# Kernel tuning notes

Hardware: AMD Instinct MI355X
Metric: run time of the kernel (lower is better)

The kernel has to match this reference:

```python
import jax, jax.numpy as jnp
import numpy as np


def setup_inputs() -> dict:
    key = jax.random.key(0)
    k1, k2 = jax.random.split(key)
    B, C, H, W = 8, 64, 64, 64
    x = jax.random.normal(k1, (B, C, H, W), dtype=jnp.float32)
    stdv = 1.0 / np.sqrt(C)
    weight = jax.random.uniform(k2, (C, C), dtype=jnp.float32, minval=-stdv, maxval=stdv)
    return {"x": x, "weight": weight}


def reference(x, weight):
    B, C, H, W = x.shape
    N = H * W
    xf = x.reshape(B, C, N)            # [B, C, N]
    g_x = jnp.transpose(xf, (0, 2, 1))  # [B, N, C] (also theta_x)
    # f[b, i, j] = sum_c x[b, c, i] * x[b, c, j]
    f = jnp.einsum('bic,bcj->bij', g_x, xf)  # [B, N, N]
    adj = jax.nn.softmax(f, axis=-1)
    support = jnp.einsum('bnc,cd->bnd', g_x, weight)  # [B, N, C]
    y = jnp.einsum('bij,bjc->bic', adj, support)      # [B, N, C]
    y = jnp.transpose(y, (0, 2, 1)).reshape(B, C, H, W)
    return y + x
```

## Files before the change

### kernel.cpp

```cpp
#include <hip/hip_runtime.h>
#include <stdint.h>


#define NTOK 4096
#define CCH  64
#define LOG2E 1.44269504088896340736f

typedef float v4f __attribute__((ext_vector_type(4)));
typedef __bf16 v8bf __attribute__((ext_vector_type(8)));
typedef unsigned short v8us __attribute__((ext_vector_type(8)));

__device__ __forceinline__ unsigned short f2bf(float f) {
    union { float f; unsigned int u; } c; c.f = f;
    unsigned int r = c.u + 0x7fffu + ((c.u >> 16) & 1u);
    return (unsigned short)(r >> 16);
}

__device__ __forceinline__ v8bf ld8(const unsigned short* p) {
    union { v8us s; v8bf b; } u;
    u.s = *(const v8us*)p;
    return u.b;
}

__device__ __forceinline__ unsigned int pkbf(float a, float b) {
    union { float f; unsigned int u; } ua, ub; ua.f = a; ub.f = b;
    return __builtin_amdgcn_perm(ub.u, ua.u, 0x07060302u);
}

__device__ __forceinline__ void gload_lds16(const void* g, void* l) {
    __builtin_amdgcn_global_load_lds(
        (const __attribute__((address_space(1))) unsigned int*)g,
        (__attribute__((address_space(3))) unsigned int*)l,
        16, 0, 0);
}

__global__ __launch_bounds__(256) void prep_kernel(
    const float* __restrict__ x,
    const float* __restrict__ w,
    unsigned short* __restrict__ xT,
    unsigned short* __restrict__ sT)
{
    __shared__ float Xf[64 * 65];
    __shared__ __align__(16) unsigned short Xb[64 * 64];

    const int tid  = threadIdx.x;
    const int lane = tid & 63;
    const int wv   = __builtin_amdgcn_readfirstlane(tid >> 6);
    const int quad = lane >> 4;
    const int l16  = lane & 15;
    const int b    = blockIdx.y;
    const int n0   = blockIdx.x * 64;

    const float* xb = x + (size_t)b * CCH * NTOK + n0 + lane;
    #pragma unroll
    for (int k = 0; k < 16; ++k) {
        const int c = wv * 16 + k;
        Xf[c * 65 + lane] = xb[(size_t)c * NTOK];
    }
    __syncthreads();

    {
        const int n  = tid >> 2;
        const int c0 = (tid & 3) * 16;
        unsigned int pk[8];
        #pragma unroll
        for (int k = 0; k < 8; ++k) {
            const float a  = Xf[(c0 + 2 * k) * 65 + n];
            const float c2 = Xf[(c0 + 2 * k + 1) * 65 + n];
            pk[k] = (unsigned int)f2bf(a) | ((unsigned int)f2bf(c2) << 16);
        }
        unsigned short* xtr = xT + ((size_t)b * NTOK + n0 + n) * CCH + c0;
        *(uint4*)(xtr)     = *(uint4*)(pk);
        *(uint4*)(xtr + 8) = *(uint4*)(pk + 4);
        const int g0 = c0 >> 3;
        *(uint4*)(Xb + (n << 6) + ((g0 ^ (n & 7)) << 3))       = *(uint4*)(pk);
        *(uint4*)(Xb + (n << 6) + (((g0 + 1) ^ (n & 7)) << 3)) = *(uint4*)(pk + 4);
    }
    __syncthreads();

    v8bf aw0[4], aw1[4];
    #pragma unroll
    for (int dt = 0; dt < 4; ++dt) {
        #pragma unroll
        for (int j = 0; j < 8; ++j) {
            aw0[dt][j] = (__bf16)w[(quad * 8 + j) * 64 + dt * 16 + l16];
            aw1[dt][j] = (__bf16)w[(quad * 8 + j + 32) * 64 + dt * 16 + l16];
        }
    }
    const int nrow = wv * 16 + l16;
    const unsigned short* xr = Xb + (nrow << 6);
    const int cc = quad ^ (nrow & 7);
    const v8bf bx0 = ld8(xr + (cc << 3));
    const v8bf bx1 = ld8(xr + ((cc ^ 4) << 3));

    unsigned short* stb = sT + (size_t)b * CCH * NTOK + n0 + wv * 16 + l16;
    #pragma unroll
    for (int dt = 0; dt < 4; ++dt) {
        v4f z; z[0]=0.f; z[1]=0.f; z[2]=0.f; z[3]=0.f;
        z = __builtin_amdgcn_mfma_f32_16x16x32_bf16(aw0[dt], bx0, z, 0, 0, 0);
        z = __builtin_amdgcn_mfma_f32_16x16x32_bf16(aw1[dt], bx1, z, 0, 0, 0);
        #pragma unroll
        for (int r = 0; r < 4; ++r)
            stb[(size_t)(dt * 16 + quad * 4 + r) * NTOK] = f2bf(z[r]);
    }
}

__global__ __launch_bounds__(256, 4) void flash_kernel(
    const unsigned short* __restrict__ xT,
    const unsigned short* __restrict__ sT,
    float* __restrict__ part_o,
    float* __restrict__ part_l,
    int nchunk, int chunk_len)
{
    __shared__ __align__(16) unsigned short Kt[64 * 64];
    __shared__ __align__(16) unsigned short Vt[64 * 64];
    __shared__ __align__(16) unsigned short Pt[4][32 * 64];

    const int tid  = threadIdx.x;
    const int w    = tid >> 6;
    const int lane = tid & 63;
    const int quad = lane >> 4;
    const int l16  = lane & 15;
    const int l7   = l16 & 7;
    const int b     = blockIdx.z;
    const int chunk = blockIdx.y;
    const int i0   = blockIdx.x * 128;
    const int irow = i0 + w * 32;
    const int jb   = chunk * chunk_len;

    const unsigned short* xTb = xT + (size_t)b * NTOK * CCH;
    const unsigned short* sTb = sT + (size_t)b * CCH * NTOK;

    const int srow = w * 8 + (lane >> 3);
    const int sc   = (lane & 7) ^ (lane >> 3);
    unsigned short* kd0 = Kt + w * 512;
    unsigned short* vd0 = Vt + w * 512;

    v8bf aq0[2], aq1[2];
    #pragma unroll
    for (int m = 0; m < 2; ++m) {
        const unsigned short* qr = xTb + (size_t)(irow + m * 16 + l16) * CCH + quad * 8;
        aq0[m] = ld8(qr);
        aq1[m] = ld8(qr + 32);
    }

    float negml2[2];
    #pragma unroll
    for (int m = 0; m < 2; ++m) {
        float msq = 0.f;
        #pragma unroll
        for (int i = 0; i < 8; ++i) {
            float e0 = (float)aq0[m][i], e1 = (float)aq1[m][i];
            msq = fmaf(e0, e0, msq);
            msq = fmaf(e1, e1, msq);
        }
        msq += __shfl_xor(msq, 16);
        msq += __shfl_xor(msq, 32);
        negml2[m] = -msq * LOG2E;
    }

    v8bf ones;
    #pragma unroll
    for (int i = 0; i < 8; ++i) ones[i] = (__bf16)1.0f;

    v4f o[2][4];
    v4f lsum[2];
    #pragma unroll
    for (int m = 0; m < 2; ++m) {
        lsum[m][0]=0.f; lsum[m][1]=0.f; lsum[m][2]=0.f; lsum[m][3]=0.f;
        #pragma unroll
        for (int ct = 0; ct < 4; ++ct) { o[m][ct][0]=0.f; o[m][ct][1]=0.f; o[m][ct][2]=0.f; o[m][ct][3]=0.f; }
    }

    unsigned short* Pw = Pt[w];
    const int phalf = (quad & 1) * 4;
    const int pgq   = quad >> 1;

    for (int jj = 0; jj < chunk_len; jj += 64) {
        const int j0 = jb + jj;

        gload_lds16(xTb + (size_t)(j0 + srow) * CCH + sc * 8,       kd0);
        gload_lds16(xTb + (size_t)(j0 + 32 + srow) * CCH + sc * 8,  kd0 + 2048);
        gload_lds16(sTb + (size_t)srow * NTOK + j0 + sc * 8,        vd0);
        gload_lds16(sTb + (size_t)(32 + srow) * NTOK + j0 + sc * 8, vd0 + 2048);
        __syncthreads();

        #pragma unroll
        for (int jt = 0; jt < 4; ++jt) {
            const int krow = 16 * jt + l16;
            const unsigned short* kb = Kt + krow * 64;
            const int c0 = quad ^ (krow & 7);
            v8bf bk0 = ld8(kb + c0 * 8);
            v8bf bk1 = ld8(kb + (c0 ^ 4) * 8);
            #pragma unroll
            for (int m = 0; m < 2; ++m) {
                v4f z; z[0]=0.f; z[1]=0.f; z[2]=0.f; z[3]=0.f;
                z = __builtin_amdgcn_mfma_f32_16x16x32_bf16(bk0, aq0[m], z, 0, 0, 0);
                z = __builtin_amdgcn_mfma_f32_16x16x32_bf16(bk1, aq1[m], z, 0, 0, 0);
                const float p0 = exp2f(fmaf(z[0], LOG2E, negml2[m]));
                const float p1 = exp2f(fmaf(z[1], LOG2E, negml2[m]));
                const float p2 = exp2f(fmaf(z[2], LOG2E, negml2[m]));
                const float p3 = exp2f(fmaf(z[3], LOG2E, negml2[m]));
                uint2 pk; pk.x = pkbf(p0, p1); pk.y = pkbf(p2, p3);
                const int pos = (2 * jt + pgq) ^ l7;
                *(uint2*)(Pw + (m * 16 + l16) * 64 + pos * 8 + phalf) = pk;
            }
        }

        v8bf pb0[2], pb1[2];
        #pragma unroll
        for (int m = 0; m < 2; ++m) {
            const unsigned short* pr = Pw + (m * 16 + l16) * 64;
            const int p0c = quad ^ l7;
            pb0[m] = ld8(pr + p0c * 8);
            pb1[m] = ld8(pr + (p0c ^ 4) * 8);
            lsum[m] = __builtin_amdgcn_mfma_f32_16x16x32_bf16(ones, pb0[m], lsum[m], 0, 0, 0);
            lsum[m] = __builtin_amdgcn_mfma_f32_16x16x32_bf16(ones, pb1[m], lsum[m], 0, 0, 0);
        }

        #pragma unroll
        for (int ct = 0; ct < 4; ++ct) {
            const int vrow = 16 * ct + l16;
            const unsigned short* vb = Vt + vrow * 64;
            const int c0 = quad ^ (vrow & 7);
            v8bf bv0 = ld8(vb + c0 * 8);
            v8bf bv1 = ld8(vb + (c0 ^ 4) * 8);
            #pragma unroll
            for (int m = 0; m < 2; ++m) {
                o[m][ct] = __builtin_amdgcn_mfma_f32_16x16x32_bf16(bv0, pb0[m], o[m][ct], 0, 0, 0);
                o[m][ct] = __builtin_amdgcn_mfma_f32_16x16x32_bf16(bv1, pb1[m], o[m][ct], 0, 0, 0);
            }
        }
        __syncthreads();
    }

    const size_t pbase = (size_t)(b * nchunk + chunk) * NTOK + irow;
    #pragma unroll
    for (int m = 0; m < 2; ++m)
        if (quad == 0) part_l[pbase + m * 16 + l16] = lsum[m][0];
    float* po = part_o + pbase * 64;
    #pragma unroll
    for (int m = 0; m < 2; ++m)
        #pragma unroll
        for (int ct = 0; ct < 4; ++ct)
            *(v4f*)(po + (size_t)(m * 16 + l16) * 64 + ct * 16 + quad * 4) = o[m][ct];
}

template <int KS_>
__global__ __launch_bounds__(256) void combine_kernel(
    const float* __restrict__ part_o,
    const float* __restrict__ part_l,
    const float* __restrict__ x,
    float* __restrict__ out)
{
    __shared__ float Of[32 * 65];
    const int tid = threadIdx.x;
    const int b = blockIdx.y;
    const int i0 = blockIdx.x * 32;

    const int row = tid >> 3;
    const int col = (tid & 7) * 8;
    float acc[8];
    #pragma unroll
    for (int k = 0; k < 8; ++k) acc[k] = 0.f;
    float lt = 0.f;

    #pragma unroll
    for (int ch = 0; ch < KS_; ++ch) {
        const size_t base = (size_t)(b * KS_ + ch) * NTOK + i0 + row;
        lt += part_l[base];
        const float* po = part_o + base * 64 + col;
        float4 v0 = *(const float4*)(po);
        float4 v1 = *(const float4*)(po + 4);
        acc[0]+=v0.x; acc[1]+=v0.y; acc[2]+=v0.z; acc[3]+=v0.w;
        acc[4]+=v1.x; acc[5]+=v1.y; acc[6]+=v1.z; acc[7]+=v1.w;
    }
    const float inv = 1.f / lt;
    #pragma unroll
    for (int k = 0; k < 8; ++k) Of[row * 65 + col + k] = acc[k] * inv;
    __syncthreads();

    const int c    = tid >> 2;
    const int part = tid & 3;
    const float* xrow = x   + ((size_t)b * CCH + c) * NTOK + i0 + part * 8;
    float*       orow = out + ((size_t)b * CCH + c) * NTOK + i0 + part * 8;
    #pragma unroll
    for (int i4 = 0; i4 < 2; ++i4) {
        float4 xv = *(const float4*)(xrow + i4 * 4);
        float4 ov;
        ov.x = Of[(part * 8 + i4 * 4 + 0) * 65 + c] + xv.x;
        ov.y = Of[(part * 8 + i4 * 4 + 1) * 65 + c] + xv.y;
        ov.z = Of[(part * 8 + i4 * 4 + 2) * 65 + c] + xv.z;
        ov.w = Of[(part * 8 + i4 * 4 + 3) * 65 + c] + xv.w;
        *(float4*)(orow + i4 * 4) = ov;
    }
}

extern "C" void kernel_launch(void* const* d_in, const int* in_sizes, int n_in,
                              void* d_out, int out_size, void* d_ws, size_t ws_size,
                              hipStream_t stream) {
    const float* x = (const float*)d_in[0];
    const float* w = (const float*)d_in[1];
    float* out = (float*)d_out;

    const size_t xT_elems = (size_t)8 * NTOK * CCH;
    unsigned short* xT = (unsigned short*)d_ws;
    unsigned short* sT = xT + xT_elems;
    char* rest = (char*)d_ws + 2 * xT_elems * sizeof(unsigned short);

    int KS = 8;
    while (KS > 1) {
        size_t need = 2 * xT_elems * sizeof(unsigned short)
                    + (size_t)KS * ((size_t)8 * NTOK * CCH * 4 + (size_t)8 * NTOK * 4);
        if (need <= ws_size) break;
        KS >>= 1;
    }
    float* part_o = (float*)rest;
    float* part_l = (float*)(rest + (size_t)KS * 8 * NTOK * CCH * 4);

    dim3 gp(64, 8);
    prep_kernel<<<gp, 256, 0, stream>>>(x, w, xT, sT);
    dim3 gf(32, KS, 8);
    flash_kernel<<<gf, 256, 0, stream>>>(xT, sT, part_o, part_l, KS, NTOK / KS);
    dim3 gc(128, 8);
    if (KS == 8)      combine_kernel<8><<<gc, 256, 0, stream>>>(part_o, part_l, x, out);
    else if (KS == 4) combine_kernel<4><<<gc, 256, 0, stream>>>(part_o, part_l, x, out);
    else if (KS == 2) combine_kernel<2><<<gc, 256, 0, stream>>>(part_o, part_l, x, out);
    else              combine_kernel<1><<<gc, 256, 0, stream>>>(part_o, part_l, x, out);
}
```

Before: 133.3 us.

## Load K/V tiles directly from global into registers, drop LDS staging and barriers

Removes the shared-memory staging of the K (xT) and V (sT) tiles and the two block-wide barriers per iteration. Each wave now reads its MFMA operands straight from global memory, relying on L1/L2 caching because all four waves read the same tiles. Launch bounds are raised to 6 blocks per SM to exploit the smaller LDS footprint. The trade-off is four times more global/L1 traffic per block in exchange for no synchronisation stalls and higher occupancy.

```diff
diff --git a/kernel.cpp b/kernel.cpp
--- a/kernel.cpp
+++ b/kernel.cpp
@@ -25,13 +25,6 @@
 __device__ __forceinline__ unsigned int pkbf(float a, float b) {
     union { float f; unsigned int u; } ua, ub; ua.f = a; ub.f = b;
     return __builtin_amdgcn_perm(ub.u, ua.u, 0x07060302u);
-}
-
-__device__ __forceinline__ void gload_lds16(const void* g, void* l) {
-    __builtin_amdgcn_global_load_lds(
-        (const __attribute__((address_space(1))) unsigned int*)g,
-        (__attribute__((address_space(3))) unsigned int*)l,
-        16, 0, 0);
 }
 
 __global__ __launch_bounds__(256) void prep_kernel(
@@ -105,15 +98,13 @@
     }
 }
 
-__global__ __launch_bounds__(256, 4) void flash_kernel(
+__global__ __launch_bounds__(256, 6) void flash_kernel(
     const unsigned short* __restrict__ xT,
     const unsigned short* __restrict__ sT,
     float* __restrict__ part_o,
     float* __restrict__ part_l,
     int nchunk, int chunk_len)
 {
-    __shared__ __align__(16) unsigned short Kt[64 * 64];
-    __shared__ __align__(16) unsigned short Vt[64 * 64];
     __shared__ __align__(16) unsigned short Pt[4][32 * 64];
 
     const int tid  = threadIdx.x;
@@ -131,11 +122,6 @@
     const unsigned short* xTb = xT + (size_t)b * NTOK * CCH;
     const unsigned short* sTb = sT + (size_t)b * CCH * NTOK;
 
-    const int srow = w * 8 + (lane >> 3);
-    const int sc   = (lane & 7) ^ (lane >> 3);
-    unsigned short* kd0 = Kt + w * 512;
-    unsigned short* vd0 = Vt + w * 512;
-
     v8bf aq0[2], aq1[2];
     #pragma unroll
     for (int m = 0; m < 2; ++m) {
@@ -179,19 +165,11 @@
     for (int jj = 0; jj < chunk_len; jj += 64) {
         const int j0 = jb + jj;
 
-        gload_lds16(xTb + (size_t)(j0 + srow) * CCH + sc * 8,       kd0);
-        gload_lds16(xTb + (size_t)(j0 + 32 + srow) * CCH + sc * 8,  kd0 + 2048);
-        gload_lds16(sTb + (size_t)srow * NTOK + j0 + sc * 8,        vd0);
-        gload_lds16(sTb + (size_t)(32 + srow) * NTOK + j0 + sc * 8, vd0 + 2048);
-        __syncthreads();
-
         #pragma unroll
         for (int jt = 0; jt < 4; ++jt) {
-            const int krow = 16 * jt + l16;
-            const unsigned short* kb = Kt + krow * 64;
-            const int c0 = quad ^ (krow & 7);
-            v8bf bk0 = ld8(kb + c0 * 8);
-            v8bf bk1 = ld8(kb + (c0 ^ 4) * 8);
+            const unsigned short* kr = xTb + (size_t)(j0 + 16 * jt + l16) * CCH + quad * 8;
+            v8bf bk0 = ld8(kr);
+            v8bf bk1 = ld8(kr + 32);
             #pragma unroll
             for (int m = 0; m < 2; ++m) {
                 v4f z; z[0]=0.f; z[1]=0.f; z[2]=0.f; z[3]=0.f;
@@ -220,18 +198,15 @@
 
         #pragma unroll
         for (int ct = 0; ct < 4; ++ct) {
-            const int vrow = 16 * ct + l16;
-            const unsigned short* vb = Vt + vrow * 64;
-            const int c0 = quad ^ (vrow & 7);
-            v8bf bv0 = ld8(vb + c0 * 8);
-            v8bf bv1 = ld8(vb + (c0 ^ 4) * 8);
+            const unsigned short* vr = sTb + (size_t)(16 * ct + l16) * NTOK + j0 + quad * 8;
+            v8bf bv0 = ld8(vr);
+            v8bf bv1 = ld8(vr + 32);
             #pragma unroll
             for (int m = 0; m < 2; ++m) {
                 o[m][ct] = __builtin_amdgcn_mfma_f32_16x16x32_bf16(bv0, pb0[m], o[m][ct], 0, 0, 0);
                 o[m][ct] = __builtin_amdgcn_mfma_f32_16x16x32_bf16(bv1, pb1[m], o[m][ct], 0, 0, 0);
             }
         }
-        __syncthreads();
     }
 
     const size_t pbase = (size_t)(b * nchunk + chunk) * NTOK + irow;
```

After: 263.4 us. 97.6% more time.
